# Performance work log

Hardware: AMD Instinct MI355X
Metric: run time of the kernel (lower is better)

Reference implementation:

```python
import jax, jax.numpy as jnp
import numpy as np

ALPHA = 0.2  # LeakyReLU negative slope
NEG_BIG = -9e15

def setup_inputs() -> dict:
    key = jax.random.key(0)
    k1, k2, k3, k4 = jax.random.split(key, 4)
    N, F_IN, F_OUT = 8192, 128, 128
    h = jax.random.normal(k1, (N, F_IN), dtype=jnp.float32)
    adj = jax.random.randint(k2, (N, N), 0, 2, dtype=jnp.int32)
    # xavier-uniform-ish params
    W = jax.random.normal(k3, (F_IN, F_OUT), dtype=jnp.float32) * (1.0 / np.sqrt(F_IN))
    a = jax.random.normal(k4, (2 * F_OUT, 1), dtype=jnp.float32) * (1.0 / np.sqrt(2 * F_OUT))
    return {"h": h, "adj": adj, "W": W, "a": a}

def reference(h, adj, W, a):
    # Wh: [N, F_OUT]
    Wh = h @ W
    F_out = Wh.shape[1]
    # a_input @ a == (Wh @ a1)_i + (Wh @ a2)_j  (same math, no N^2*2F tensor)
    a1 = a[:F_out, 0]   # [F_OUT]
    a2 = a[F_out:, 0]   # [F_OUT]
    e = (Wh @ a1)[:, None] + (Wh @ a2)[None, :]        # [N, N]
    e = jnp.where(e >= 0, e, ALPHA * e)                # LeakyReLU(0.2)
    scores = jnp.where(adj > 0, e, NEG_BIG)
    attention = jax.nn.softmax(scores, axis=1)         # row-wise
    # dropout skipped (eval mode / training=False)
    return attention @ Wh                              # [N, F_OUT]
```

## Files before the change

kernel.cpp:

```cpp
#include <hip/hip_runtime.h>
#include <hip/hip_bf16.h>

#define N 8192
#define FD 128
#define LOG2E 1.4426950408889634f

typedef __attribute__((ext_vector_type(4))) float f4;
typedef __attribute__((ext_vector_type(4))) int i32x4;
typedef __attribute__((ext_vector_type(4))) unsigned int u32x4;
typedef __attribute__((ext_vector_type(8))) __bf16 bf16x8;

__device__ __forceinline__ unsigned short bfbits(float x){
  __bf16 b = (__bf16)x;
  return __builtin_bit_cast(unsigned short, b);
}

__global__ __launch_bounds__(256) void k12_wh(const float* __restrict__ h,
                                              const float* __restrict__ W,
                                              const float* __restrict__ a,
                                              unsigned short* __restrict__ Bsw,
                                              float* __restrict__ s1L,
                                              float* __restrict__ s2L){
  __shared__ float Wl[64*128];
  __shared__ float hT[128*33];
  int t = threadIdx.x;
  int i0 = blockIdx.x * 32;
  {
    int r  = t >> 3;
    int k0 = (t & 7) * 16;
    const f4* src = (const f4*)&h[(size_t)(i0 + r)*FD + k0];
    #pragma unroll
    for (int q = 0; q < 4; ++q){
      f4 v = src[q];
      #pragma unroll
      for (int e = 0; e < 4; ++e) hT[(k0 + q*4 + e)*33 + r] = v[e];
    }
  }
  int f0 = (t & 31) * 4;
  int r0 = (t >> 5) * 4;
  float acc[4][4] = {};
  for (int half = 0; half < 2; ++half){
    __syncthreads();
    #pragma unroll
    for (int v = 0; v < 8; ++v){
      int idx = (v*256 + t)*4;
      *(f4*)&Wl[idx] = *(const f4*)&W[half*8192 + idx];
    }
    __syncthreads();
    for (int k2 = 0; k2 < 64; ++k2){
      f4 wv = *(const f4*)&Wl[k2*FD + f0];
      f4 hv = *(const f4*)&hT[(half*64 + k2)*33 + r0];
      #pragma unroll
      for (int ri = 0; ri < 4; ++ri)
        #pragma unroll
        for (int fi = 0; fi < 4; ++fi)
          acc[ri][fi] = __builtin_fmaf(hv[ri], wv[fi], acc[ri][fi]);
    }
  }
  int jblk = blockIdx.x;
  int n  = f0 >> 4;
  int fl = f0 & 15;
  #pragma unroll
  for (int ri = 0; ri < 4; ++ri){
    int k = r0 + ri;
    size_t base = (((size_t)jblk*8 + n)*64 + ((k>>3)<<4))*8 + (k&7);
    #pragma unroll
    for (int fi = 0; fi < 4; ++fi)
      Bsw[base + (size_t)(fl + fi)*8] = bfbits(acc[ri][fi]);
  }
  f4 a1v = *(const f4*)&a[f0];
  f4 a2v = *(const f4*)&a[FD + f0];
  float p1[4], p2[4];
  #pragma unroll
  for (int ri = 0; ri < 4; ++ri){
    p1[ri] = 0.f; p2[ri] = 0.f;
    #pragma unroll
    for (int fi = 0; fi < 4; ++fi){
      p1[ri] = __builtin_fmaf(acc[ri][fi], a1v[fi], p1[ri]);
      p2[ri] = __builtin_fmaf(acc[ri][fi], a2v[fi], p2[ri]);
    }
  }
  #pragma unroll
  for (int d = 1; d < 32; d <<= 1){
    #pragma unroll
    for (int ri = 0; ri < 4; ++ri){
      p1[ri] += __shfl_xor(p1[ri], d, 32);
      p2[ri] += __shfl_xor(p2[ri], d, 32);
    }
  }
  if ((t & 31) == 0){
    #pragma unroll
    for (int ri = 0; ri < 4; ++ri){
      s1L[i0 + r0 + ri] = p1[ri] * LOG2E;
      s2L[i0 + r0 + ri] = p2[ri] * LOG2E;
    }
  }
}

__global__ __launch_bounds__(256) void k3_max(const float* __restrict__ s2L,
                                              float* __restrict__ M2L){
  __shared__ float red[4];
  int t = threadIdx.x;
  float m = -3.0e38f;
  for (int i = t; i < N; i += 256) m = fmaxf(m, s2L[i]);
  #pragma unroll
  for (int d = 1; d < 64; d <<= 1) m = fmaxf(m, __shfl_xor(m, d, 64));
  if ((t & 63) == 0) red[t >> 6] = m;
  __syncthreads();
  if (t == 0) *M2L = fmaxf(fmaxf(red[0], red[1]), fmaxf(red[2], red[3]));
}

__global__ __launch_bounds__(256,2) void k4_flash(const int* __restrict__ adj,
    const unsigned short* __restrict__ Bsw,
    const float* __restrict__ s1L, const float* __restrict__ s2L,
    const float* __restrict__ M2p,
    float* __restrict__ partial, float* __restrict__ denomp, int njc){
  __shared__ __align__(16) unsigned char bswl[2][32768];
  __shared__ __align__(16) unsigned char mknib[2][128*32];
  __shared__ __align__(16) float s2l[2][128];
  int t = threadIdx.x;
  int wv = t >> 6, lane = t & 63;
  int lrow = lane & 15, lgrp = lane >> 4;
  int bid = blockIdx.x;
  int y  = bid & (njc - 1);
  int bx = bid / njc;
  int jlen = N / njc;
  int jstart = y * jlen;
  int nmac = jlen >> 7;
  float M2 = *M2p;
  int i0w = bx*128 + wv*32;
  float s1a = s1L[i0w + lrow], s1b = s1L[i0w + 16 + lrow];
  float ea = s1a + M2, eb = s1b + M2;
  float maL = fmaxf(ea, 0.2f*ea);
  float mbL = fmaxf(eb, 0.2f*eb);

  f4 acc[2][8]; f4 accd[2];
  #pragma unroll
  for (int x = 0; x < 2; ++x){
    accd[x] = (f4){0.f,0.f,0.f,0.f};
    #pragma unroll
    for (int n = 0; n < 8; ++n) acc[x][n] = (f4){0.f,0.f,0.f,0.f};
  }
  u32x4 onesbits = (u32x4){0x3F803F80u,0x3F803F80u,0x3F803F80u,0x3F803F80u};
  bf16x8 ones = __builtin_bit_cast(bf16x8, onesbits);

  const i32x4* adj4 = (const i32x4*)adj;
  int sr2 = lane >> 5;
  int sj  = lane & 31;
  size_t abase = ((size_t)(bx*128 + wv*32 + sr2) * N) >> 2;

  i32x4 st[16];

  #define STAGE_BSW(jb0, b) do {                                               \
    const unsigned int* bg = (const unsigned int*)(Bsw + (size_t)((jb0) >> 5) * 4096); \
    _Pragma("unroll")                                                          \
    for (int q = 0; q < 8; ++q){                                               \
      int chunk = q*4 + wv;                                                    \
      __builtin_amdgcn_global_load_lds(                                        \
        (const __attribute__((address_space(1))) unsigned int*)(bg + (size_t)(chunk*64 + lane)*4), \
        (__attribute__((address_space(3))) unsigned int*)(&bswl[b][0] + chunk*1024), \
        16, 0, 0);                                                             \
    }                                                                          \
  } while(0)

  #define STAGE_ADJ(jb0) do {                                                  \
    size_t ab = abase + (size_t)((jb0) >> 2) + sj;                             \
    _Pragma("unroll")                                                          \
    for (int e = 0; e < 16; ++e) st[e] = adj4[ab + (size_t)e * 4096];          \
  } while(0)

  #define PACK_MASKS(b) do {                                                   \
    _Pragma("unroll")                                                          \
    for (int e = 0; e < 16; ++e){                                              \
      unsigned nib = (st[e][0] != 0 ? 1u : 0u) | (st[e][1] != 0 ? 2u : 0u)     \
                   | (st[e][2] != 0 ? 4u : 0u) | (st[e][3] != 0 ? 8u : 0u);    \
      int rloc = wv*32 + e*2 + sr2;                                            \
      mknib[b][rloc*32 + sj] = (unsigned char)nib;                             \
    }                                                                          \
  } while(0)

  int buf = 0;
  STAGE_BSW(jstart, 0);
  STAGE_ADJ(jstart);
  PACK_MASKS(0);
  if (t < 32) *(f4*)&s2l[0][t*4] = *(const f4*)&s2L[jstart + t*4];
  __syncthreads();

  for (int m = 0; m < nmac; ++m){
    int jb0 = jstart + m*128;
    if (m + 1 < nmac){
      STAGE_BSW(jb0 + 128, buf ^ 1);
      STAGE_ADJ(jb0 + 128);
    }
    #pragma unroll
    for (int js = 0; js < 4; ++js){
      int jo = js*32 + lgrp*8;
      f4 ya = *(const f4*)&s2l[buf][jo];
      f4 yb = *(const f4*)&s2l[buf][jo+4];
      int gb = (js*4 + lgrp)*2;
      unsigned short ua = *(const unsigned short*)&mknib[buf][(wv*32 + lrow)*32 + gb];
      unsigned short ub = *(const unsigned short*)&mknib[buf][(wv*32 + 16 + lrow)*32 + gb];
      unsigned mba = (ua & 0xFu) | ((ua >> 4) & 0xF0u);
      unsigned mbb = (ub & 0xFu) | ((ub >> 4) & 0xF0u);
      bf16x8 fa, fb;
      #pragma unroll
      for (int e = 0; e < 8; ++e){
        float sjv = (e < 4) ? ya[e] : yb[e-4];
        float xa = s1a + sjv,            xb = s1b + sjv;
        float la = fmaxf(xa, 0.2f*xa),   lb = fmaxf(xb, 0.2f*xb);
        float pa = ((mba>>e)&1u) ? __builtin_amdgcn_exp2f(la - maL) : 0.f;
        float pb = ((mbb>>e)&1u) ? __builtin_amdgcn_exp2f(lb - mbL) : 0.f;
        fa[e] = (__bf16)pa; fb[e] = (__bf16)pb;
      }
      accd[0] = __builtin_amdgcn_mfma_f32_16x16x32_bf16(fa, ones, accd[0], 0, 0, 0);
      accd[1] = __builtin_amdgcn_mfma_f32_16x16x32_bf16(fb, ones, accd[1], 0, 0, 0);
      {
        u32x4 b0[4];
        #pragma unroll
        for (int n = 0; n < 4; ++n)
          b0[n] = *(const u32x4*)&bswl[buf][((js*8 + n)*64 + lane)*16];
        #pragma unroll
        for (int n = 0; n < 4; ++n){
          bf16x8 bb = __builtin_bit_cast(bf16x8, b0[n]);
          acc[0][n] = __builtin_amdgcn_mfma_f32_16x16x32_bf16(fa, bb, acc[0][n], 0, 0, 0);
          acc[1][n] = __builtin_amdgcn_mfma_f32_16x16x32_bf16(fb, bb, acc[1][n], 0, 0, 0);
        }
      }
      {
        u32x4 b1[4];
        #pragma unroll
        for (int n = 0; n < 4; ++n)
          b1[n] = *(const u32x4*)&bswl[buf][((js*8 + 4 + n)*64 + lane)*16];
        #pragma unroll
        for (int n = 0; n < 4; ++n){
          bf16x8 bb = __builtin_bit_cast(bf16x8, b1[n]);
          acc[0][4+n] = __builtin_amdgcn_mfma_f32_16x16x32_bf16(fa, bb, acc[0][4+n], 0, 0, 0);
          acc[1][4+n] = __builtin_amdgcn_mfma_f32_16x16x32_bf16(fb, bb, acc[1][4+n], 0, 0, 0);
        }
      }
    }
    if (m + 1 < nmac){
      PACK_MASKS(buf ^ 1);
      if (t < 32) *(f4*)&s2l[buf ^ 1][t*4] = *(const f4*)&s2L[jb0 + 128 + t*4];
    }
    __syncthreads();
    buf ^= 1;
  }

  if (lrow == 0){
    #pragma unroll
    for (int x = 0; x < 2; ++x)
      #pragma unroll
      for (int r = 0; r < 4; ++r)
        denomp[(size_t)y*N + i0w + x*16 + lgrp*4 + r] = accd[x][r];
  }
  float* pb = partial + (size_t)y * N * FD;
  #pragma unroll
  for (int x = 0; x < 2; ++x)
    #pragma unroll
    for (int n = 0; n < 8; ++n)
      #pragma unroll
      for (int r = 0; r < 4; ++r)
        pb[(size_t)(i0w + x*16 + lgrp*4 + r)*FD + n*16 + lrow] = acc[x][n][r];
}

__global__ __launch_bounds__(256) void k5_fin(const float* __restrict__ partial,
    const float* __restrict__ denomp, float* __restrict__ out, int njc){
  int g = blockIdx.x*256 + threadIdx.x;
  int i = g >> 7;
  float num = 0.f, den = 0.f;
  for (int c = 0; c < njc; ++c) num += partial[(size_t)c*N*FD + g];
  for (int c = 0; c < njc; ++c) den += denomp[(size_t)c*N + i];
  out[g] = num / den;
}

extern "C" void kernel_launch(void* const* d_in, const int* in_sizes, int n_in,
                              void* d_out, int out_size, void* d_ws, size_t ws_size,
                              hipStream_t stream){
  const float* h   = (const float*)d_in[0];
  const int*   adj = (const int*)d_in[1];
  const float* W   = (const float*)d_in[2];
  const float* a   = (const float*)d_in[3];
  float* out = (float*)d_out;
  char* ws = (char*)d_ws;

  unsigned short* Bsw = (unsigned short*)ws;
  float* s1L = (float*)(ws + (size_t)(6u<<20));
  float* s2L = (float*)(ws + (size_t)(6u<<20) + 32768);
  float* M2L = (float*)(ws + (size_t)(6u<<20) + 65536);
  float* denomp  = (float*)(ws + (size_t)(7u<<20));
  float* partial = (float*)(ws + (size_t)(8u<<20));

  size_t chunk = (size_t)N * FD * sizeof(float);
  int njc = 1;
  if (ws_size > ((size_t)(8u<<20))){
    size_t m = (ws_size - (size_t)(8u<<20)) / chunk;
    njc = (m >= 8) ? 8 : (m >= 4) ? 4 : (m >= 2) ? 2 : 1;
  }

  hipLaunchKernelGGL(k12_wh, dim3(256), dim3(256), 0, stream, h, W, a, Bsw, s1L, s2L);
  hipLaunchKernelGGL(k3_max, dim3(1),   dim3(256), 0, stream, s2L, M2L);
  hipLaunchKernelGGL(k4_flash, dim3(64*njc), dim3(256), 0, stream,
                     adj, Bsw, s1L, s2L, M2L, partial, denomp, njc);
  hipLaunchKernelGGL(k5_fin, dim3(N*FD/256), dim3(256), 0, stream, partial, denomp, out, njc);
}
```

Measured before the change: 402.3 us.

## Restructure flash kernel: batch adj mask packing per 1024-column segment, smaller tiles

The adjacency mask is no longer loaded and packed per 128-column step. Each block now loads a whole 1024-column segment of adj with wide coalesced loads, packs it into a padded bitmask in LDS, and then runs 16 inner steps of 64 columns with double-buffered Wh tiles. LDS and register use are cut (smaller Bsw buffers, no staging registers) so launch bounds can request 3 blocks per CU instead of 2. The trade-off is that the adj load phase is serialized before compute within each segment rather than overlapped, and barriers become more frequent.

New measurement: 429.9 us. 6.9% more time.

```diff
diff --git a/kernel.cpp b/kernel.cpp
--- a/kernel.cpp
+++ b/kernel.cpp
@@ -4,6 +4,7 @@
 #define N 8192
 #define FD 128
 #define LOG2E 1.4426950408889634f
+#define CMS 132
 
 typedef __attribute__((ext_vector_type(4))) float f4;
 typedef __attribute__((ext_vector_type(4))) int i32x4;
@@ -110,14 +111,14 @@
   if (t == 0) *M2L = fmaxf(fmaxf(red[0], red[1]), fmaxf(red[2], red[3]));
 }
 
-__global__ __launch_bounds__(256,2) void k4_flash(const int* __restrict__ adj,
+__global__ __launch_bounds__(256,3) void k4_flash(const int* __restrict__ adj,
     const unsigned short* __restrict__ Bsw,
     const float* __restrict__ s1L, const float* __restrict__ s2L,
     const float* __restrict__ M2p,
     float* __restrict__ partial, float* __restrict__ denomp, int njc){
-  __shared__ __align__(16) unsigned char bswl[2][32768];
-  __shared__ __align__(16) unsigned char mknib[2][128*32];
-  __shared__ __align__(16) float s2l[2][128];
+  __shared__ __align__(16) unsigned char bswl[2][16384];
+  __shared__ __align__(16) unsigned char cmask[128*CMS];
+  __shared__ __align__(16) float s2l[2][64];
   int t = threadIdx.x;
   int wv = t >> 6, lane = t & 63;
   int lrow = lane & 15, lgrp = lane >> 4;
@@ -126,7 +127,7 @@
   int bx = bid / njc;
   int jlen = N / njc;
   int jstart = y * jlen;
-  int nmac = jlen >> 7;
+  int nseg = jlen >> 10;
   float M2 = *M2p;
   int i0w = bx*128 + wv*32;
   float s1a = s1L[i0w + lrow], s1b = s1L[i0w + 16 + lrow];
@@ -134,27 +135,14 @@
   float maL = fmaxf(ea, 0.2f*ea);
   float mbL = fmaxf(eb, 0.2f*eb);
 
-  f4 acc[2][8]; f4 accd[2];
-  #pragma unroll
-  for (int x = 0; x < 2; ++x){
-    accd[x] = (f4){0.f,0.f,0.f,0.f};
-    #pragma unroll
-    for (int n = 0; n < 8; ++n) acc[x][n] = (f4){0.f,0.f,0.f,0.f};
-  }
   u32x4 onesbits = (u32x4){0x3F803F80u,0x3F803F80u,0x3F803F80u,0x3F803F80u};
   bf16x8 ones = __builtin_bit_cast(bf16x8, onesbits);
-
   const i32x4* adj4 = (const i32x4*)adj;
-  int sr2 = lane >> 5;
-  int sj  = lane & 31;
-  size_t abase = ((size_t)(bx*128 + wv*32 + sr2) * N) >> 2;
-
-  i32x4 st[16];
-
-  #define STAGE_BSW(jb0, b) do {                                               \
+
+  #define STAGE_BSW64(jb0, b) do {                                             \
     const unsigned int* bg = (const unsigned int*)(Bsw + (size_t)((jb0) >> 5) * 4096); \
     _Pragma("unroll")                                                          \
-    for (int q = 0; q < 8; ++q){                                               \
+    for (int q = 0; q < 4; ++q){                                               \
       int chunk = q*4 + wv;                                                    \
       __builtin_amdgcn_global_load_lds(                                        \
         (const __attribute__((address_space(1))) unsigned int*)(bg + (size_t)(chunk*64 + lane)*4), \
@@ -163,88 +151,110 @@
     }                                                                          \
   } while(0)
 
-  #define STAGE_ADJ(jb0) do {                                                  \
-    size_t ab = abase + (size_t)((jb0) >> 2) + sj;                             \
-    _Pragma("unroll")                                                          \
-    for (int e = 0; e < 16; ++e) st[e] = adj4[ab + (size_t)e * 4096];          \
-  } while(0)
-
-  #define PACK_MASKS(b) do {                                                   \
-    _Pragma("unroll")                                                          \
-    for (int e = 0; e < 16; ++e){                                              \
-      unsigned nib = (st[e][0] != 0 ? 1u : 0u) | (st[e][1] != 0 ? 2u : 0u)     \
-                   | (st[e][2] != 0 ? 4u : 0u) | (st[e][3] != 0 ? 8u : 0u);    \
-      int rloc = wv*32 + e*2 + sr2;                                            \
-      mknib[b][rloc*32 + sj] = (unsigned char)nib;                             \
-    }                                                                          \
-  } while(0)
-
-  int buf = 0;
-  STAGE_BSW(jstart, 0);
-  STAGE_ADJ(jstart);
-  PACK_MASKS(0);
-  if (t < 32) *(f4*)&s2l[0][t*4] = *(const f4*)&s2L[jstart + t*4];
-  __syncthreads();
-
-  for (int m = 0; m < nmac; ++m){
-    int jb0 = jstart + m*128;
-    if (m + 1 < nmac){
-      STAGE_BSW(jb0 + 128, buf ^ 1);
-      STAGE_ADJ(jb0 + 128);
-    }
-    #pragma unroll
-    for (int js = 0; js < 4; ++js){
-      int jo = js*32 + lgrp*8;
-      f4 ya = *(const f4*)&s2l[buf][jo];
-      f4 yb = *(const f4*)&s2l[buf][jo+4];
-      int gb = (js*4 + lgrp)*2;
-      unsigned short ua = *(const unsigned short*)&mknib[buf][(wv*32 + lrow)*32 + gb];
-      unsigned short ub = *(const unsigned short*)&mknib[buf][(wv*32 + 16 + lrow)*32 + gb];
-      unsigned mba = (ua & 0xFu) | ((ua >> 4) & 0xF0u);
-      unsigned mbb = (ub & 0xFu) | ((ub >> 4) & 0xF0u);
-      bf16x8 fa, fb;
-      #pragma unroll
-      for (int e = 0; e < 8; ++e){
-        float sjv = (e < 4) ? ya[e] : yb[e-4];
-        float xa = s1a + sjv,            xb = s1b + sjv;
-        float la = fmaxf(xa, 0.2f*xa),   lb = fmaxf(xb, 0.2f*xb);
-        float pa = ((mba>>e)&1u) ? __builtin_amdgcn_exp2f(la - maL) : 0.f;
-        float pb = ((mbb>>e)&1u) ? __builtin_amdgcn_exp2f(lb - mbL) : 0.f;
-        fa[e] = (__bf16)pa; fb[e] = (__bf16)pb;
+  f4 acc[2][8]; f4 accd[2];
+  #pragma unroll
+  for (int x = 0; x < 2; ++x){
+    accd[x] = (f4){0.f,0.f,0.f,0.f};
+    #pragma unroll
+    for (int n = 0; n < 8; ++n) acc[x][n] = (f4){0.f,0.f,0.f,0.f};
+  }
+
+  int crowA = wv*32 + lrow;
+  int crowB = crowA + 16;
+
+  for (int seg = 0; seg < nseg; ++seg){
+    int segj = jstart + seg*1024;
+    if (seg > 0) __syncthreads();
+    {
+      size_t rb4 = (((size_t)(bx*128 + wv*32)) * 2048) + (size_t)(segj >> 2);
+      for (int rb = 0; rb < 8; ++rb){
+        i32x4 ld[4][4];
+        #pragma unroll
+        for (int rr = 0; rr < 4; ++rr){
+          size_t base = rb4 + (size_t)(rb*4 + rr)*2048;
+          ld[rr][0] = adj4[base + lane*2];
+          ld[rr][1] = adj4[base + lane*2 + 1];
+          ld[rr][2] = adj4[base + 128 + lane*2];
+          ld[rr][3] = adj4[base + 128 + lane*2 + 1];
+        }
+        #pragma unroll
+        for (int rr = 0; rr < 4; ++rr){
+          int crow = wv*32 + rb*4 + rr;
+          unsigned b0 = 0, b1 = 0;
+          #pragma unroll
+          for (int e = 0; e < 4; ++e){
+            b0 |= (ld[rr][0][e] != 0 ? 1u : 0u) << e;
+            b0 |= (ld[rr][1][e] != 0 ? 1u : 0u) << (4+e);
+            b1 |= (ld[rr][2][e] != 0 ? 1u : 0u) << e;
+            b1 |= (ld[rr][3][e] != 0 ? 1u : 0u) << (4+e);
+          }
+          int w0 = lane, w1 = 64 + lane;
+          cmask[crow*CMS + (w0&3)*32 + ((w0>>3)&15)*2 + ((w0>>2)&1)] = (unsigned char)b0;
+          cmask[crow*CMS + (w1&3)*32 + ((w1>>3)&15)*2 + ((w1>>2)&1)] = (unsigned char)b1;
+        }
       }
-      accd[0] = __builtin_amdgcn_mfma_f32_16x16x32_bf16(fa, ones, accd[0], 0, 0, 0);
-      accd[1] = __builtin_amdgcn_mfma_f32_16x16x32_bf16(fb, ones, accd[1], 0, 0, 0);
-      {
-        u32x4 b0[4];
+    }
+    __syncthreads();
+    int buf = 0;
+    STAGE_BSW64(segj, 0);
+    if (t < 16) *(f4*)&s2l[0][t*4] = *(const f4*)&s2L[segj + t*4];
+    __syncthreads();
+    for (int m = 0; m < 16; ++m){
+      int jb0 = segj + m*64;
+      if (m < 15){
+        STAGE_BSW64(jb0 + 64, buf ^ 1);
+        if (t < 16) *(f4*)&s2l[buf ^ 1][t*4] = *(const f4*)&s2L[jb0 + 64 + t*4];
+      }
+      int moff = lgrp*32 + m*2;
+      unsigned ua = *(const unsigned short*)&cmask[crowA*CMS + moff];
+      unsigned ub = *(const unsigned short*)&cmask[crowB*CMS + moff];
+      #pragma unroll
+      for (int js = 0; js < 2; ++js){
+        int jo = js*32 + lgrp*8;
+        f4 ya = *(const f4*)&s2l[buf][jo];
+        f4 yb = *(const f4*)&s2l[buf][jo+4];
+        unsigned mba = (ua >> (js*8)) & 0xFFu;
+        unsigned mbb = (ub >> (js*8)) & 0xFFu;
+        bf16x8 fa, fb;
         #pragma unroll
-        for (int n = 0; n < 4; ++n)
-          b0[n] = *(const u32x4*)&bswl[buf][((js*8 + n)*64 + lane)*16];
-        #pragma unroll
-        for (int n = 0; n < 4; ++n){
-          bf16x8 bb = __builtin_bit_cast(bf16x8, b0[n]);
-          acc[0][n] = __builtin_amdgcn_mfma_f32_16x16x32_bf16(fa, bb, acc[0][n], 0, 0, 0);
-          acc[1][n] = __builtin_amdgcn_mfma_f32_16x16x32_bf16(fb, bb, acc[1][n], 0, 0, 0);
+        for (int e = 0; e < 8; ++e){
+          float sjv = (e < 4) ? ya[e] : yb[e-4];
+          float xa = s1a + sjv,            xb = s1b + sjv;
+          float la = fmaxf(xa, 0.2f*xa),   lb = fmaxf(xb, 0.2f*xb);
+          float pa = ((mba>>e)&1u) ? __builtin_amdgcn_exp2f(la - maL) : 0.f;
+          float pb = ((mbb>>e)&1u) ? __builtin_amdgcn_exp2f(lb - mbL) : 0.f;
+          fa[e] = (__bf16)pa; fb[e] = (__bf16)pb;
+        }
+        accd[0] = __builtin_amdgcn_mfma_f32_16x16x32_bf16(fa, ones, accd[0], 0, 0, 0);
+        accd[1] = __builtin_amdgcn_mfma_f32_16x16x32_bf16(fb, ones, accd[1], 0, 0, 0);
+        {
+          u32x4 b0[4];
+          #pragma unroll
+          for (int n = 0; n < 4; ++n)
+            b0[n] = *(const u32x4*)&bswl[buf][((js*8 + n)*64 + lane)*16];
+          #pragma unroll
+          for (int n = 0; n < 4; ++n){
+            bf16x8 bb = __builtin_bit_cast(bf16x8, b0[n]);
+            acc[0][n] = __builtin_amdgcn_mfma_f32_16x16x32_bf16(fa, bb, acc[0][n], 0, 0, 0);
+            acc[1][n] = __builtin_amdgcn_mfma_f32_16x16x32_bf16(fb, bb, acc[1][n], 0, 0, 0);
+          }
+        }
+        {
+          u32x4 b1[4];
+          #pragma unroll
+          for (int n = 0; n < 4; ++n)
+            b1[n] = *(const u32x4*)&bswl[buf][((js*8 + 4 + n)*64 + lane)*16];
+          #pragma unroll
+          for (int n = 0; n < 4; ++n){
+            bf16x8 bb = __builtin_bit_cast(bf16x8, b1[n]);
+            acc[0][4+n] = __builtin_amdgcn_mfma_f32_16x16x32_bf16(fa, bb, acc[0][4+n], 0, 0, 0);
+            acc[1][4+n] = __builtin_amdgcn_mfma_f32_16x16x32_bf16(fb, bb, acc[1][4+n], 0, 0, 0);
+          }
         }
       }
-      {
-        u32x4 b1[4];
-        #pragma unroll
-        for (int n = 0; n < 4; ++n)
-          b1[n] = *(const u32x4*)&bswl[buf][((js*8 + 4 + n)*64 + lane)*16];
-        #pragma unroll
-        for (int n = 0; n < 4; ++n){
-          bf16x8 bb = __builtin_bit_cast(bf16x8, b1[n]);
-          acc[0][4+n] = __builtin_amdgcn_mfma_f32_16x16x32_bf16(fa, bb, acc[0][4+n], 0, 0, 0);
-          acc[1][4+n] = __builtin_amdgcn_mfma_f32_16x16x32_bf16(fb, bb, acc[1][4+n], 0, 0, 0);
-        }
-      }
-    }
-    if (m + 1 < nmac){
-      PACK_MASKS(buf ^ 1);
-      if (t < 32) *(f4*)&s2l[buf ^ 1][t*4] = *(const f4*)&s2L[jb0 + 128 + t*4];
-    }
-    __syncthreads();
-    buf ^= 1;
+      __syncthreads();
+      buf ^= 1;
+    }
   }
 
   if (lrow == 0){
```

## Precompress adjacency into bitmask kernel and stage whole mask slice in LDS

Applied to the files above, without the earlier changes.

Adds a separate pre-pass that packs the int32 adjacency matrix into a bit-per-entry mask. The attention kernel then loads its whole mask slice into LDS once, instead of streaming and packing adj in its main loop. The main loop step shrinks to 64 columns, so the Bsw double buffer and LDS footprint get smaller, launch bounds rise to 3 blocks per CU, and s2 values are read straight from global. The aim is to take the heavy adj traffic and packing work out of the compute loop. In exchange it adds a kernel launch and a mask write/read round trip, and it hardcodes njc=8, which assumes the workspace is large enough.

Result: slower. 441.5 us (+9.7%).

```diff
diff --git a/kernel.cpp b/kernel.cpp
--- a/kernel.cpp
+++ b/kernel.cpp
@@ -4,6 +4,7 @@
 #define N 8192
 #define FD 128
 #define LOG2E 1.4426950408889634f
+#define CMSTR 144
 
 typedef __attribute__((ext_vector_type(4))) float f4;
 typedef __attribute__((ext_vector_type(4))) int i32x4;
@@ -13,6 +14,21 @@
 __device__ __forceinline__ unsigned short bfbits(float x){
   __bf16 b = (__bf16)x;
   return __builtin_bit_cast(unsigned short, b);
+}
+
+__global__ __launch_bounds__(256) void kc_compress(const int* __restrict__ adj,
+                                                   unsigned char* __restrict__ cmask){
+  int tid = blockIdx.x*256 + threadIdx.x;
+  const int TOT = 2048*256;
+  const i32x4* adj4 = (const i32x4*)adj;
+  #pragma unroll 4
+  for (int k = 0; k < 16; ++k){
+    size_t g = (size_t)tid + (size_t)k*TOT;
+    i32x4 a = adj4[g*2], b = adj4[g*2+1];
+    unsigned v = (a[0]!=0?1u:0u) | (a[1]!=0?2u:0u) | (a[2]!=0?4u:0u) | (a[3]!=0?8u:0u)
+               | (b[0]!=0?16u:0u)| (b[1]!=0?32u:0u)| (b[2]!=0?64u:0u)| (b[3]!=0?128u:0u);
+    cmask[g] = (unsigned char)v;
+  }
 }
 
 __global__ __launch_bounds__(256) void k12_wh(const float* __restrict__ h,
@@ -110,14 +126,13 @@
   if (t == 0) *M2L = fmaxf(fmaxf(red[0], red[1]), fmaxf(red[2], red[3]));
 }
 
-__global__ __launch_bounds__(256,2) void k4_flash(const int* __restrict__ adj,
+__global__ __launch_bounds__(256,3) void k4_flash(const unsigned char* __restrict__ cmask,
     const unsigned short* __restrict__ Bsw,
     const float* __restrict__ s1L, const float* __restrict__ s2L,
     const float* __restrict__ M2p,
     float* __restrict__ partial, float* __restrict__ denomp, int njc){
-  __shared__ __align__(16) unsigned char bswl[2][32768];
-  __shared__ __align__(16) unsigned char mknib[2][128*32];
-  __shared__ __align__(16) float s2l[2][128];
+  __shared__ __align__(16) unsigned char bswl[2][16384];
+  __shared__ __align__(16) unsigned char cml[128*CMSTR];
   int t = threadIdx.x;
   int wv = t >> 6, lane = t & 63;
   int lrow = lane & 15, lgrp = lane >> 4;
@@ -126,7 +141,7 @@
   int bx = bid / njc;
   int jlen = N / njc;
   int jstart = y * jlen;
-  int nmac = jlen >> 7;
+  int nmac = jlen >> 6;
   float M2 = *M2p;
   int i0w = bx*128 + wv*32;
   float s1a = s1L[i0w + lrow], s1b = s1L[i0w + 16 + lrow];
@@ -143,18 +158,12 @@
   }
   u32x4 onesbits = (u32x4){0x3F803F80u,0x3F803F80u,0x3F803F80u,0x3F803F80u};
   bf16x8 ones = __builtin_bit_cast(bf16x8, onesbits);
-
-  const i32x4* adj4 = (const i32x4*)adj;
-  int sr2 = lane >> 5;
-  int sj  = lane & 31;
-  size_t abase = ((size_t)(bx*128 + wv*32 + sr2) * N) >> 2;
-
-  i32x4 st[16];
-
-  #define STAGE_BSW(jb0, b) do {                                               \
+  const f4* s2v = (const f4*)s2L;
+
+  #define STAGE_BSW64(jb0, b) do {                                             \
     const unsigned int* bg = (const unsigned int*)(Bsw + (size_t)((jb0) >> 5) * 4096); \
     _Pragma("unroll")                                                          \
-    for (int q = 0; q < 8; ++q){                                               \
+    for (int q = 0; q < 4; ++q){                                               \
       int chunk = q*4 + wv;                                                    \
       __builtin_amdgcn_global_load_lds(                                        \
         (const __attribute__((address_space(1))) unsigned int*)(bg + (size_t)(chunk*64 + lane)*4), \
@@ -163,45 +172,32 @@
     }                                                                          \
   } while(0)
 
-  #define STAGE_ADJ(jb0) do {                                                  \
-    size_t ab = abase + (size_t)((jb0) >> 2) + sj;                             \
-    _Pragma("unroll")                                                          \
-    for (int e = 0; e < 16; ++e) st[e] = adj4[ab + (size_t)e * 4096];          \
-  } while(0)
-
-  #define PACK_MASKS(b) do {                                                   \
-    _Pragma("unroll")                                                          \
-    for (int e = 0; e < 16; ++e){                                              \
-      unsigned nib = (st[e][0] != 0 ? 1u : 0u) | (st[e][1] != 0 ? 2u : 0u)     \
-                   | (st[e][2] != 0 ? 4u : 0u) | (st[e][3] != 0 ? 8u : 0u);    \
-      int rloc = wv*32 + e*2 + sr2;                                            \
-      mknib[b][rloc*32 + sj] = (unsigned char)nib;                             \
-    }                                                                          \
-  } while(0)
+  {
+    int rr = t >> 1, hb = (t & 1) * 64;
+    const unsigned char* src = cmask + (size_t)(bx*128 + rr)*(N/8) + (jstart >> 3) + hb;
+    #pragma unroll
+    for (int q = 0; q < 4; ++q){
+      u32x4 v = *(const u32x4*)(src + q*16);
+      *(u32x4*)&cml[rr*CMSTR + hb + q*16] = v;
+    }
+  }
 
   int buf = 0;
-  STAGE_BSW(jstart, 0);
-  STAGE_ADJ(jstart);
-  PACK_MASKS(0);
-  if (t < 32) *(f4*)&s2l[0][t*4] = *(const f4*)&s2L[jstart + t*4];
+  STAGE_BSW64(jstart, 0);
   __syncthreads();
 
+  int rA = (wv*32 + lrow)*CMSTR;
+  int rB = (wv*32 + 16 + lrow)*CMSTR;
   for (int m = 0; m < nmac; ++m){
-    int jb0 = jstart + m*128;
-    if (m + 1 < nmac){
-      STAGE_BSW(jb0 + 128, buf ^ 1);
-      STAGE_ADJ(jb0 + 128);
-    }
-    #pragma unroll
-    for (int js = 0; js < 4; ++js){
-      int jo = js*32 + lgrp*8;
-      f4 ya = *(const f4*)&s2l[buf][jo];
-      f4 yb = *(const f4*)&s2l[buf][jo+4];
-      int gb = (js*4 + lgrp)*2;
-      unsigned short ua = *(const unsigned short*)&mknib[buf][(wv*32 + lrow)*32 + gb];
-      unsigned short ub = *(const unsigned short*)&mknib[buf][(wv*32 + 16 + lrow)*32 + gb];
-      unsigned mba = (ua & 0xFu) | ((ua >> 4) & 0xF0u);
-      unsigned mbb = (ub & 0xFu) | ((ub >> 4) & 0xF0u);
+    int jb0 = jstart + m*64;
+    if (m + 1 < nmac) STAGE_BSW64(jb0 + 64, buf ^ 1);
+    #pragma unroll
+    for (int js = 0; js < 2; ++js){
+      int jb = jb0 + js*32 + lgrp*8;
+      f4 ya = s2v[jb >> 2], yb = s2v[(jb >> 2) + 1];
+      int cb = m*8 + js*4 + lgrp;
+      unsigned mba = cml[rA + cb];
+      unsigned mbb = cml[rB + cb];
       bf16x8 fa, fb;
       #pragma unroll
       for (int e = 0; e < 8; ++e){
@@ -239,10 +235,6 @@
         }
       }
     }
-    if (m + 1 < nmac){
-      PACK_MASKS(buf ^ 1);
-      if (t < 32) *(f4*)&s2l[buf ^ 1][t*4] = *(const f4*)&s2L[jb0 + 128 + t*4];
-    }
     __syncthreads();
     buf ^= 1;
   }
@@ -290,17 +282,14 @@
   float* M2L = (float*)(ws + (size_t)(6u<<20) + 65536);
   float* denomp  = (float*)(ws + (size_t)(7u<<20));
   float* partial = (float*)(ws + (size_t)(8u<<20));
-
-  size_t chunk = (size_t)N * FD * sizeof(float);
-  int njc = 1;
-  if (ws_size > ((size_t)(8u<<20))){
-    size_t m = (ws_size - (size_t)(8u<<20)) / chunk;
-    njc = (m >= 8) ? 8 : (m >= 4) ? 4 : (m >= 2) ? 2 : 1;
-  }
-
+  unsigned char* cmask = (unsigned char*)(ws + (size_t)(40u<<20));
+
+  const int njc = 8;
+
+  hipLaunchKernelGGL(kc_compress, dim3(2048), dim3(256), 0, stream, adj, cmask);
   hipLaunchKernelGGL(k12_wh, dim3(256), dim3(256), 0, stream, h, W, a, Bsw, s1L, s2L);
   hipLaunchKernelGGL(k3_max, dim3(1),   dim3(256), 0, stream, s2L, M2L);
   hipLaunchKernelGGL(k4_flash, dim3(64*njc), dim3(256), 0, stream,
-                     adj, Bsw, s1L, s2L, M2L, partial, denomp, njc);
+                     cmask, Bsw, s1L, s2L, M2L, partial, denomp, njc);
   hipLaunchKernelGGL(k5_fin, dim3(N*FD/256), dim3(256), 0, stream, partial, denomp, out, njc);
 }
```
